# Optimization experiments

Measured on AMD Instinct MI355X. Metric: run time of the kernel, lower is better.

The kernel has to match this reference:

```python
import jax, jax.numpy as jnp
import numpy as np

N, D, K = 32768, 256, 4096
COMMITMENT_COST = 0.25
EPS_NORM = 1e-12  # matches torch F.normalize eps


def _l2_normalize(x):
    n = jnp.linalg.norm(x, axis=1, keepdims=True)
    return x / jnp.maximum(n, EPS_NORM)


def setup_inputs() -> dict:
    key = jax.random.key(0)
    k1, k2 = jax.random.split(key)
    inputs = jax.random.normal(k1, (N, D), dtype=jnp.float32)
    # xavier_uniform-like scale for the codebook
    bound = float(np.sqrt(6.0 / (K + D)))
    embeddings = jax.random.uniform(k2, (K, D), dtype=jnp.float32, minval=-bound, maxval=bound)
    return {"inputs": inputs, "embeddings": embeddings}


def reference(inputs, embeddings):
    flat = inputs.reshape(-1, D)
    x = _l2_normalize(flat)              # [N, D]
    e = _l2_normalize(embeddings)        # [K, D]
    # squared euclidean distance on normalized vectors
    distances = (jnp.sum(x * x, axis=1, keepdims=True)
                 + jnp.sum(e * e, axis=1)
                 - 2.0 * jnp.matmul(x, e.T))          # [N, K]
    encoding_indices = jnp.argmin(distances, axis=1)  # [N]
    quantized = embeddings[encoding_indices]          # gather, [N, D]
    # commitment loss (EMA variant: only commitment term is trained)
    e_latent_loss = jnp.mean((jax.lax.stop_gradient(quantized) - flat) ** 2)
    loss = COMMITMENT_COST * e_latent_loss
    # straight-through estimator
    quantized_st = flat + jax.lax.stop_gradient(quantized - flat)
    quantized_st = quantized_st.reshape(inputs.shape)
    return quantized_st, loss, encoding_indices
```

## Files before the change

kernel.cpp:

```cpp
#include <hip/hip_runtime.h>
#include <math.h>
#include <stdint.h>
#include <limits.h>

#define NPTS 32768
#define DIM  256
#define KCB  4096
#define NQ   (NPTS*DIM)

#define EPSN    1e-12f
#define MARGIN1 6.0e-4f
#define F16MIN  6.103515625e-05f
#define CAPB    4096
#define KINIT   0x7F800000FFFFFFFFull

typedef __attribute__((ext_vector_type(8))) _Float16 f16x8;
typedef __attribute__((ext_vector_type(4))) _Float16 f16x4;
typedef __attribute__((ext_vector_type(4))) float    f32x4;

#define WS_EH0   0u
#define WS_TRI   2097152u
#define WS_SUME  4194304u
#define WS_EINV  4210688u
#define WS_XINV  4227072u
#define WS_IDX   4358144u
#define WS_RCA   4489216u
#define WS_RLA   4489232u
#define WS_RCB   4751376u
#define WS_RLB   4751392u
#define WS_BEST  4882464u
#define WS_LOSSP 4915232u

__device__ inline unsigned fbits(float f){ union{float f;unsigned u;}v; v.f=f; return v.u; }
__device__ inline float bitsf(unsigned u){ union{float f;unsigned u;}v; v.u=u; return v.f; }
__device__ inline uint64_t dbits(double d){ union{double d;uint64_t u;}v; v.d=d; return v.u; }
__device__ inline _Float16 g16(float v){
    return (fabsf(v) < F16MIN) ? (_Float16)0.0f : (_Float16)v;
}
__device__ inline void gload16(const void* src, void* lds){
    __builtin_amdgcn_global_load_lds((const __attribute__((address_space(1))) void*)src,
                                     (__attribute__((address_space(3))) void*)lds, 16, 0, 0);
}

__global__ __launch_bounds__(256) void k_norm_x(const float* __restrict__ x,
                                                float* __restrict__ xinv) {
    int w = threadIdx.x >> 6, l = threadIdx.x & 63;
    int row = blockIdx.x * 4 + w;
    float4 v = ((const float4*)x)[row * 64 + l];
    float s = v.x*v.x + v.y*v.y + v.z*v.z + v.w*v.w;
    #pragma unroll
    for (int o = 32; o; o >>= 1) s += __shfl_xor(s, o);
    if (l == 0) xinv[row] = 1.0f / fmaxf(sqrtf(s), EPSN);
}

__global__ __launch_bounds__(256) void k_norm_e(const float* __restrict__ e,
                                                _Float16* __restrict__ eh0,
                                                float* __restrict__ sume,
                                                float* __restrict__ einv,
                                                int* __restrict__ rca,
                                                int* __restrict__ rcb,
                                                uint64_t* __restrict__ bestu) {
    if (blockIdx.x == 0 && threadIdx.x == 0) { *rca = 0; *rcb = 0; }
    if (blockIdx.x < 16) bestu[blockIdx.x * 256 + threadIdx.x] = ~0ull;
    int w = threadIdx.x >> 6, l = threadIdx.x & 63;
    int row = blockIdx.x * 4 + w;
    float4 v = ((const float4*)e)[row * 64 + l];
    float s = v.x*v.x + v.y*v.y + v.z*v.z + v.w*v.w;
    #pragma unroll
    for (int o = 32; o; o >>= 1) s += __shfl_xor(s, o);
    float inv = 1.0f / fmaxf(sqrtf(s), EPSN);
    float4 n = make_float4(v.x*inv, v.y*inv, v.z*inv, v.w*inv);
    f16x4 h0; h0[0]=g16(n.x); h0[1]=g16(n.y); h0[2]=g16(n.z); h0[3]=g16(n.w);
    ((f16x4*)eh0)[row * 64 + l] = h0;
    float s2 = n.x*n.x + n.y*n.y + n.z*n.z + n.w*n.w;
    #pragma unroll
    for (int o = 32; o; o >>= 1) s2 += __shfl_xor(s2, o);
    if (l == 0) { sume[row] = s2; einv[row] = inv; }
}

__global__ __launch_bounds__(256,2) void k_phase1(
    const float* __restrict__ x, const float* __restrict__ xinv,
    const _Float16* __restrict__ eh0,
    ulonglong2* __restrict__ tri)
{
    __shared__ __align__(16) _Float16 Bs[2][32 * DIM];
    const int tid = threadIdx.x;
    const int w = tid >> 6, l = tid & 63;
    const int l15 = l & 15, lhi = l >> 4;
    const int rowbase = (blockIdx.x >> 2) * 256 + w * 64;
    const int kbase   = (blockIdx.x & 3) * 1024;
    char* BsC = (char*)&Bs[0][0];

    f16x8 a[4][8];
    #pragma unroll
    for (int g = 0; g < 4; g++) {
        int row = rowbase + g*16 + l15;
        float xv = xinv[row];
        const float4* xr = (const float4*)(x + row * DIM);
        #pragma unroll
        for (int dc = 0; dc < 8; dc++) {
            float4 f0 = xr[dc*8 + lhi*2];
            float4 f1 = xr[dc*8 + lhi*2 + 1];
            f16x8 av;
            av[0]=g16(f0.x*xv); av[1]=g16(f0.y*xv);
            av[2]=g16(f0.z*xv); av[3]=g16(f0.w*xv);
            av[4]=g16(f1.x*xv); av[5]=g16(f1.y*xv);
            av[6]=g16(f1.z*xv); av[7]=g16(f1.w*xv);
            a[g][dc] = av;
        }
    }

    uint64_t t0[4], t1[4];
    float d2[4];
    #pragma unroll
    for (int g = 0; g < 4; g++) { t0[g]=KINIT; t1[g]=KINIT; d2[g]=INFINITY; }

    const char* sbase = (const char*)eh0 + (size_t)kbase * 512
                      + (size_t)(l & 31) * 512 + w*32 + (l >> 5)*16;
    auto stage = [&](int kt, int bufbyte) {
        const char* s = sbase + kt * 16384;
        #pragma unroll
        for (int p = 0; p < 4; p++) {
            gload16(s + p*128, BsC + bufbyte + ((p*256 + w*64) << 4));
        }
    };

    const int rb = lhi*512 + l15*16;
    const f32x4 zc = (f32x4){0.f, 0.f, 0.f, 0.f};

    auto compute = [&](int kt, int bufbyte) {
        f32x4 acc[4][2];
        #pragma unroll
        for (int dc = 0; dc < 8; dc++) {
            #pragma unroll
            for (int ni = 0; ni < 2; ni++) {
                f16x8 b = *(const f16x8*)(BsC + bufbyte + dc*2048 + ni*256 + rb);
                if (dc == 0) {
                    acc[0][ni] = __builtin_amdgcn_mfma_f32_16x16x32_f16(b, a[0][0], zc, 0, 0, 0);
                    acc[1][ni] = __builtin_amdgcn_mfma_f32_16x16x32_f16(b, a[1][0], zc, 0, 0, 0);
                    acc[2][ni] = __builtin_amdgcn_mfma_f32_16x16x32_f16(b, a[2][0], zc, 0, 0, 0);
                    acc[3][ni] = __builtin_amdgcn_mfma_f32_16x16x32_f16(b, a[3][0], zc, 0, 0, 0);
                } else {
                    acc[0][ni] = __builtin_amdgcn_mfma_f32_16x16x32_f16(b, a[0][dc], acc[0][ni], 0, 0, 0);
                    acc[1][ni] = __builtin_amdgcn_mfma_f32_16x16x32_f16(b, a[1][dc], acc[1][ni], 0, 0, 0);
                    acc[2][ni] = __builtin_amdgcn_mfma_f32_16x16x32_f16(b, a[2][dc], acc[2][ni], 0, 0, 0);
                    acc[3][ni] = __builtin_amdgcn_mfma_f32_16x16x32_f16(b, a[3][dc], acc[3][ni], 0, 0, 0);
                }
            }
        }

        #pragma unroll
        for (int ni = 0; ni < 2; ni++) {
            #pragma unroll
            for (int g = 0; g < 4; g++) {
                f32x4 v = acc[g][ni];
                float mx = fmaxf(fmaxf(v[0], v[1]), fmaxf(v[2], v[3]));
                if (5.0f - 2.0f*mx < d2[g]) {
                    #pragma unroll
                    for (int r = 0; r < 4; r++) {
                        float db = 5.0f - 2.0f*v[r];
                        if (db < d2[g]) {
                            int code = kbase + kt*32 + ni*16 + lhi*4 + r;
                            uint64_t key = ((uint64_t)fbits(db) << 32) | (unsigned)code;
                            if (key < t1[g]) {
                                d2[g] = bitsf((unsigned)(t1[g] >> 32));
                                if (key < t0[g]) { t1[g] = t0[g]; t0[g] = key; }
                                else t1[g] = key;
                            } else {
                                d2[g] = db;
                            }
                        }
                    }
                }
            }
        }
    };

    stage(0, 0);
    for (int kt = 0; kt < 32; kt += 2) {
        __syncthreads();
        stage(kt + 1, 16384);
        compute(kt, 0);
        __syncthreads();
        if (kt + 2 < 32) stage(kt + 2, 0);
        compute(kt + 1, 16384);
    }

    #pragma unroll
    for (int g = 0; g < 4; g++) {
        uint64_t a0 = t0[g], a1 = t1[g];
        float a2 = d2[g];
        #pragma unroll
        for (int m = 16; m < 64; m <<= 1) {
            uint64_t b0 = __shfl_xor(a0, m), b1 = __shfl_xor(a1, m);
            float    b2 = __shfl_xor(a2, m);
            uint64_t lo  = a0 < b0 ? a0 : b0;
            uint64_t hi0 = a0 < b0 ? b0 : a0;
            uint64_t lo1 = a1 < b1 ? a1 : b1;
            uint64_t mid = hi0 > lo1 ? hi0 : lo1;
            a1 = hi0 < lo1 ? hi0 : lo1;
            a0 = lo;
            a2 = fminf(fminf(a2, b2), bitsf((unsigned)(mid >> 32)));
        }
        t0[g] = a0; t1[g] = a1; d2[g] = a2;
    }

    if (lhi == 0) {
        const int split = blockIdx.x & 3;
        #pragma unroll
        for (int g = 0; g < 4; g++) {
            int row = rowbase + g*16 + l15;
            float d0 = bitsf((unsigned)(t0[g] >> 32));
            uint64_t flag = (d2[g] - d0 < MARGIN1) ? (1ull << 12) : 0ull;
            ulonglong2 ent;
            ent.x = t0[g];
            ent.y = t1[g] | flag;
            tri[(row << 2) | split] = ent;
        }
    }
}

__global__ __launch_bounds__(256) void k_merge(
    const ulonglong2* __restrict__ tri,
    int* __restrict__ idx,
    int* __restrict__ rca, int2* __restrict__ rla,
    int* __restrict__ rcb, int* __restrict__ rlb)
{
    int row = blockIdx.x * 256 + threadIdx.x;
    ulonglong2 e0 = tri[row*4 + 0];
    ulonglong2 e1 = tri[row*4 + 1];
    ulonglong2 e2 = tri[row*4 + 2];
    ulonglong2 e3 = tri[row*4 + 3];

    uint64_t c0 = e0.x, c1 = e0.y & ~0x1000ull;
    float c2 = INFINITY;
    auto fold = [&](uint64_t b0, uint64_t b1) {
        b1 &= ~0x1000ull;
        uint64_t lo  = c0 < b0 ? c0 : b0;
        uint64_t hi0 = c0 < b0 ? b0 : c0;
        uint64_t lo1 = c1 < b1 ? c1 : b1;
        uint64_t mid = hi0 > lo1 ? hi0 : lo1;
        c1 = hi0 < lo1 ? hi0 : lo1;
        c0 = lo;
        c2 = fminf(c2, bitsf((unsigned)(mid >> 32)));
    };
    fold(e1.x, e1.y);
    fold(e2.x, e2.y);
    fold(e3.x, e3.y);

    int k0 = (int)((unsigned)c0 & 0xFFFu);
    idx[row] = k0;
    float d0 = bitsf((unsigned)(c0 >> 32));
    float d1 = bitsf((unsigned)(c1 >> 32));
    bool lA = (d1 - d0 < MARGIN1);
    bool lB = (c2 - d0 < MARGIN1);
    if ((e0.y >> 12) & 1) lB |= (bitsf((unsigned)(e0.x >> 32)) - d0 < MARGIN1);
    if ((e1.y >> 12) & 1) lB |= (bitsf((unsigned)(e1.x >> 32)) - d0 < MARGIN1);
    if ((e2.y >> 12) & 1) lB |= (bitsf((unsigned)(e2.x >> 32)) - d0 < MARGIN1);
    if ((e3.y >> 12) & 1) lB |= (bitsf((unsigned)(e3.x >> 32)) - d0 < MARGIN1);

    if (lA) {
        int k1 = (int)((unsigned)c1 & 0xFFFu);
        int p = atomicAdd(rca, 1);
        if (p < NPTS) rla[p] = make_int2(row, k0 | (k1 << 12));
    }
    if (lB) {
        int q = atomicAdd(rcb, 1);
        if (q < CAPB) rlb[q] = row;
    }
}

__global__ __launch_bounds__(256) void k_cand(
    const float* __restrict__ x, const float* __restrict__ emb,
    const float* __restrict__ xinv, const float* __restrict__ einv,
    const float* __restrict__ sume,
    const int* __restrict__ rca, const int2* __restrict__ rla,
    int* __restrict__ idx)
{
    int cnt = *rca; if (cnt > NPTS) cnt = NPTS;
    const int w = threadIdx.x >> 6, l = threadIdx.x & 63;
    for (int r = blockIdx.x * 4 + w; r < cnt; r += gridDim.x * 4) {
        int2 ent = rla[r];
        int row = ent.x;
        int k0 = ent.y & 0xFFF, k1 = (ent.y >> 12) & 0xFFF;
        float xv = xinv[row];
        float4 xf = ((const float4*)x)[row * 64 + l];
        double x0 = (double)xf.x * (double)xv, x1 = (double)xf.y * (double)xv;
        double x2 = (double)xf.z * (double)xv, x3 = (double)xf.w * (double)xv;
        int ks[2] = {k0, k1};
        double d[2];
        #pragma unroll
        for (int c = 0; c < 2; c++) {
            int k = ks[c];
            float ev = einv[k];
            float4 e4 = ((const float4*)emb)[k * 64 + l];
            d[c] = x0 * (double)(e4.x * ev) + x1 * (double)(e4.y * ev)
                 + x2 * (double)(e4.z * ev) + x3 * (double)(e4.w * ev);
        }
        #pragma unroll
        for (int o = 32; o; o >>= 1) {
            d[0] += __shfl_xor(d[0], o);
            d[1] += __shfl_xor(d[1], o);
        }
        if (l == 0) {
            double dist0 = 4.0 + (double)sume[k0] - 2.0 * d[0];
            double dist1 = 4.0 + (double)sume[k1] - 2.0 * d[1];
            uint64_t key0 = (dbits(dist0) & 0xFFFFFFFFFFFFF000ull) | (unsigned)k0;
            uint64_t key1 = (dbits(dist1) & 0xFFFFFFFFFFFFF000ull) | (unsigned)k1;
            idx[row] = (int)((key0 < key1 ? key0 : key1) & 0xFFFull);
        }
    }
}

__global__ __launch_bounds__(256) void k_full(
    const float* __restrict__ x, const float* __restrict__ emb,
    const float* __restrict__ xinv, const float* __restrict__ einv,
    const float* __restrict__ sume,
    const int* __restrict__ rcb, const int* __restrict__ rlb,
    uint64_t* __restrict__ bestu)
{
    __shared__ __align__(16) float xs[DIM];
    int cnt = *rcb; if (cnt > CAPB) cnt = CAPB; if (cnt <= 0) return;
    const int tid = threadIdx.x;
    const int grp = tid >> 3, sub = tid & 7;
    int items = cnt * 16;
    for (int item = blockIdx.x; item < items; item += gridDim.x) {
        int r = item >> 4, chunk = item & 15;
        int row = rlb[r];
        __syncthreads();
        xs[tid] = x[row * DIM + tid] * xinv[row];
        __syncthreads();
        const float4* xs4 = (const float4*)xs;
        uint64_t best = ~0ull;
        #pragma unroll
        for (int j = 0; j < 8; j++) {
            int k = chunk * 256 + grp * 8 + j;
            float ev = einv[k];
            const float4* e4 = (const float4*)(emb + k * DIM);
            double dp = 0;
            #pragma unroll
            for (int i = 0; i < 8; i++) {
                float4 ef = e4[sub + i*8];
                float4 xf = xs4[sub + i*8];
                dp += (double)xf.x * (double)(ef.x * ev)
                    + (double)xf.y * (double)(ef.y * ev)
                    + (double)xf.z * (double)(ef.z * ev)
                    + (double)xf.w * (double)(ef.w * ev);
            }
            #pragma unroll
            for (int o = 4; o; o >>= 1) dp += __shfl_xor(dp, o);
            if (sub == 0) {
                double dist = 4.0 + (double)sume[k] - 2.0 * dp;
                uint64_t key = (dbits(dist) & 0xFFFFFFFFFFFFF000ull) | (unsigned)k;
                best = key < best ? key : best;
            }
        }
        if (sub == 0)
            atomicMin((unsigned long long*)&bestu[r], (unsigned long long)best);
    }
}

__global__ __launch_bounds__(256) void k_ffin(const int* __restrict__ rcb,
                                              const int* __restrict__ rlb,
                                              const uint64_t* __restrict__ bestu,
                                              int* __restrict__ idx) {
    int cnt = *rcb; if (cnt > CAPB) cnt = CAPB;
    int i = blockIdx.x * 256 + threadIdx.x;
    if (i < cnt) idx[rlb[i]] = (int)(bestu[i] & 0xFFFull);
}

__global__ __launch_bounds__(256) void k_gather(const float* __restrict__ x,
                                                const float* __restrict__ emb,
                                                const int* __restrict__ idx,
                                                float* __restrict__ out,
                                                float* __restrict__ lossp) {
    int t = blockIdx.x * 256 + threadIdx.x;
    float ls = 0.f;
    #pragma unroll
    for (int s = 0; s < 4; ++s) {
        int i4 = t + s * 524288;
        int n = i4 >> 6, c4 = i4 & 63;
        int id = idx[n];
        float4 f = ((const float4*)x)[i4];
        float4 q = ((const float4*)emb)[id * 64 + c4];
        float dx = q.x - f.x, dy = q.y - f.y, dz = q.z - f.z, dw = q.w - f.w;
        float4 o = make_float4(f.x + dx, f.y + dy, f.z + dz, f.w + dw);
        ((float4*)out)[i4] = o;
        ls += dx*dx + dy*dy + dz*dz + dw*dw;
        if (c4 == 0) out[NQ + 1 + n] = (float)id;
    }
    #pragma unroll
    for (int o = 32; o; o >>= 1) ls += __shfl_xor(ls, o);
    __shared__ float wsum[4];
    int wid = threadIdx.x >> 6, lane = threadIdx.x & 63;
    if (lane == 0) wsum[wid] = ls;
    __syncthreads();
    if (threadIdx.x == 0) lossp[blockIdx.x] = wsum[0] + wsum[1] + wsum[2] + wsum[3];
}

__global__ __launch_bounds__(256) void k_finalize(const float* __restrict__ lossp,
                                                  float* __restrict__ out) {
    double s = 0;
    for (int i = threadIdx.x; i < 2048; i += 256) s += (double)lossp[i];
    #pragma unroll
    for (int o = 32; o; o >>= 1) s += __shfl_xor(s, o);
    __shared__ double wd[4];
    int wid = threadIdx.x >> 6, lane = threadIdx.x & 63;
    if (lane == 0) wd[wid] = s;
    __syncthreads();
    if (threadIdx.x == 0)
        out[NQ] = (float)(0.25 * ((wd[0] + wd[1] + wd[2] + wd[3]) / (double)NQ));
}

extern "C" void kernel_launch(void* const* d_in, const int* in_sizes, int n_in,
                              void* d_out, int out_size, void* d_ws, size_t ws_size,
                              hipStream_t stream) {
    const float* x   = (const float*)d_in[0];
    const float* emb = (const float*)d_in[1];
    char* ws = (char*)d_ws;
    _Float16* eh0 = (_Float16*)(ws + WS_EH0);
    ulonglong2* tri = (ulonglong2*)(ws + WS_TRI);
    float* sume  = (float*)(ws + WS_SUME);
    float* einv  = (float*)(ws + WS_EINV);
    float* xinv  = (float*)(ws + WS_XINV);
    int*   idx   = (int*)  (ws + WS_IDX);
    int*   rca   = (int*)  (ws + WS_RCA);
    int2*  rla   = (int2*) (ws + WS_RLA);
    int*   rcb   = (int*)  (ws + WS_RCB);
    int*   rlb   = (int*)  (ws + WS_RLB);
    uint64_t* bestu = (uint64_t*)(ws + WS_BEST);
    float* lossp = (float*)(ws + WS_LOSSP);
    float* out = (float*)d_out;

    hipLaunchKernelGGL(k_norm_x,   dim3(NPTS/4),     dim3(256), 0, stream, x, xinv);
    hipLaunchKernelGGL(k_norm_e,   dim3(KCB/4),      dim3(256), 0, stream,
                       emb, eh0, sume, einv, rca, rcb, bestu);
    hipLaunchKernelGGL(k_phase1,   dim3(NPTS/256*4), dim3(256), 0, stream,
                       x, xinv, eh0, tri);
    hipLaunchKernelGGL(k_merge,    dim3(NPTS/256),   dim3(256), 0, stream,
                       tri, idx, rca, rla, rcb, rlb);
    hipLaunchKernelGGL(k_cand,     dim3(1024),       dim3(256), 0, stream,
                       x, emb, xinv, einv, sume, rca, rla, idx);
    hipLaunchKernelGGL(k_full,     dim3(2048),       dim3(256), 0, stream,
                       x, emb, xinv, einv, sume, rcb, rlb, bestu);
    hipLaunchKernelGGL(k_ffin,     dim3(16),         dim3(256), 0, stream, rcb, rlb, bestu, idx);
    hipLaunchKernelGGL(k_gather,   dim3(2048),       dim3(256), 0, stream,
                       x, emb, idx, out, lossp);
    hipLaunchKernelGGL(k_finalize, dim3(1),          dim3(256), 0, stream, lossp, out);
}
```

Measured before the change: 177.8 us.

## Fuse merge, candidate rescoring and full-rescan kernels into one block-local tail kernel

```diff
diff --git a/kernel.cpp b/kernel.cpp
--- a/kernel.cpp
+++ b/kernel.cpp
@@ -11,7 +11,6 @@
 #define EPSN    1e-12f
 #define MARGIN1 6.0e-4f
 #define F16MIN  6.103515625e-05f
-#define CAPB    4096
 #define KINIT   0x7F800000FFFFFFFFull
 
 typedef __attribute__((ext_vector_type(8))) _Float16 f16x8;
@@ -24,11 +23,6 @@
 #define WS_EINV  4210688u
 #define WS_XINV  4227072u
 #define WS_IDX   4358144u
-#define WS_RCA   4489216u
-#define WS_RLA   4489232u
-#define WS_RCB   4751376u
-#define WS_RLB   4751392u
-#define WS_BEST  4882464u
 #define WS_LOSSP 4915232u
 
 __device__ inline unsigned fbits(float f){ union{float f;unsigned u;}v; v.f=f; return v.u; }
@@ -56,12 +50,7 @@
 __global__ __launch_bounds__(256) void k_norm_e(const float* __restrict__ e,
                                                 _Float16* __restrict__ eh0,
                                                 float* __restrict__ sume,
-                                                float* __restrict__ einv,
-                                                int* __restrict__ rca,
-                                                int* __restrict__ rcb,
-                                                uint64_t* __restrict__ bestu) {
-    if (blockIdx.x == 0 && threadIdx.x == 0) { *rca = 0; *rcb = 0; }
-    if (blockIdx.x < 16) bestu[blockIdx.x * 256 + threadIdx.x] = ~0ull;
+                                                float* __restrict__ einv) {
     int w = threadIdx.x >> 6, l = threadIdx.x & 63;
     int row = blockIdx.x * 4 + w;
     float4 v = ((const float4*)e)[row * 64 + l];
@@ -220,69 +209,65 @@
     }
 }
 
-__global__ __launch_bounds__(256) void k_merge(
+__global__ __launch_bounds__(256) void k_tail(
     const ulonglong2* __restrict__ tri,
-    int* __restrict__ idx,
-    int* __restrict__ rca, int2* __restrict__ rla,
-    int* __restrict__ rcb, int* __restrict__ rlb)
-{
-    int row = blockIdx.x * 256 + threadIdx.x;
-    ulonglong2 e0 = tri[row*4 + 0];
-    ulonglong2 e1 = tri[row*4 + 1];
-    ulonglong2 e2 = tri[row*4 + 2];
-    ulonglong2 e3 = tri[row*4 + 3];
-
-    uint64_t c0 = e0.x, c1 = e0.y & ~0x1000ull;
-    float c2 = INFINITY;
-    auto fold = [&](uint64_t b0, uint64_t b1) {
-        b1 &= ~0x1000ull;
-        uint64_t lo  = c0 < b0 ? c0 : b0;
-        uint64_t hi0 = c0 < b0 ? b0 : c0;
-        uint64_t lo1 = c1 < b1 ? c1 : b1;
-        uint64_t mid = hi0 > lo1 ? hi0 : lo1;
-        c1 = hi0 < lo1 ? hi0 : lo1;
-        c0 = lo;
-        c2 = fminf(c2, bitsf((unsigned)(mid >> 32)));
-    };
-    fold(e1.x, e1.y);
-    fold(e2.x, e2.y);
-    fold(e3.x, e3.y);
-
-    int k0 = (int)((unsigned)c0 & 0xFFFu);
-    idx[row] = k0;
-    float d0 = bitsf((unsigned)(c0 >> 32));
-    float d1 = bitsf((unsigned)(c1 >> 32));
-    bool lA = (d1 - d0 < MARGIN1);
-    bool lB = (c2 - d0 < MARGIN1);
-    if ((e0.y >> 12) & 1) lB |= (bitsf((unsigned)(e0.x >> 32)) - d0 < MARGIN1);
-    if ((e1.y >> 12) & 1) lB |= (bitsf((unsigned)(e1.x >> 32)) - d0 < MARGIN1);
-    if ((e2.y >> 12) & 1) lB |= (bitsf((unsigned)(e2.x >> 32)) - d0 < MARGIN1);
-    if ((e3.y >> 12) & 1) lB |= (bitsf((unsigned)(e3.x >> 32)) - d0 < MARGIN1);
-
-    if (lA) {
-        int k1 = (int)((unsigned)c1 & 0xFFFu);
-        int p = atomicAdd(rca, 1);
-        if (p < NPTS) rla[p] = make_int2(row, k0 | (k1 << 12));
-    }
-    if (lB) {
-        int q = atomicAdd(rcb, 1);
-        if (q < CAPB) rlb[q] = row;
-    }
-}
-
-__global__ __launch_bounds__(256) void k_cand(
     const float* __restrict__ x, const float* __restrict__ emb,
     const float* __restrict__ xinv, const float* __restrict__ einv,
     const float* __restrict__ sume,
-    const int* __restrict__ rca, const int2* __restrict__ rla,
     int* __restrict__ idx)
 {
-    int cnt = *rca; if (cnt > NPTS) cnt = NPTS;
-    const int w = threadIdx.x >> 6, l = threadIdx.x & 63;
-    for (int r = blockIdx.x * 4 + w; r < cnt; r += gridDim.x * 4) {
-        int2 ent = rla[r];
-        int row = ent.x;
-        int k0 = ent.y & 0xFFF, k1 = (ent.y >> 12) & 0xFFF;
+    __shared__ int rowsA[256], ksA[256], rowsB[256];
+    __shared__ int cntA, cntB;
+    __shared__ __align__(16) float xs[DIM];
+    __shared__ uint64_t sk[32];
+    const int tid = threadIdx.x;
+    if (tid == 0) { cntA = 0; cntB = 0; }
+    __syncthreads();
+
+    {
+        int row = blockIdx.x * 256 + tid;
+        ulonglong2 e0 = tri[row*4+0], e1 = tri[row*4+1],
+                   e2 = tri[row*4+2], e3 = tri[row*4+3];
+        uint64_t c0 = e0.x, c1 = e0.y & ~0x1000ull;
+        float c2 = INFINITY;
+        auto fold = [&](uint64_t b0, uint64_t b1) {
+            b1 &= ~0x1000ull;
+            uint64_t lo  = c0 < b0 ? c0 : b0;
+            uint64_t hi0 = c0 < b0 ? b0 : c0;
+            uint64_t lo1 = c1 < b1 ? c1 : b1;
+            uint64_t mid = hi0 > lo1 ? hi0 : lo1;
+            c1 = hi0 < lo1 ? hi0 : lo1;
+            c0 = lo;
+            c2 = fminf(c2, bitsf((unsigned)(mid >> 32)));
+        };
+        fold(e1.x, e1.y); fold(e2.x, e2.y); fold(e3.x, e3.y);
+        int k0 = (int)((unsigned)c0 & 0xFFFu);
+        idx[row] = k0;
+        float d0 = bitsf((unsigned)(c0 >> 32));
+        float d1 = bitsf((unsigned)(c1 >> 32));
+        bool lA = (d1 - d0 < MARGIN1);
+        bool lB = (c2 - d0 < MARGIN1);
+        if ((e0.y >> 12) & 1) lB |= (bitsf((unsigned)(e0.x >> 32)) - d0 < MARGIN1);
+        if ((e1.y >> 12) & 1) lB |= (bitsf((unsigned)(e1.x >> 32)) - d0 < MARGIN1);
+        if ((e2.y >> 12) & 1) lB |= (bitsf((unsigned)(e2.x >> 32)) - d0 < MARGIN1);
+        if ((e3.y >> 12) & 1) lB |= (bitsf((unsigned)(e3.x >> 32)) - d0 < MARGIN1);
+        if (lA) {
+            int k1 = (int)((unsigned)c1 & 0xFFFu);
+            int p = atomicAdd(&cntA, 1);
+            rowsA[p] = row; ksA[p] = k0 | (k1 << 12);
+        }
+        if (lB) {
+            int q = atomicAdd(&cntB, 1);
+            rowsB[q] = row;
+        }
+    }
+    __syncthreads();
+
+    const int w = tid >> 6, l = tid & 63;
+    const int nA = cntA;
+    for (int i = w; i < nA; i += 4) {
+        int row = rowsA[i];
+        int k0 = ksA[i] & 0xFFF, k1 = (ksA[i] >> 12) & 0xFFF;
         float xv = xinv[row];
         float4 xf = ((const float4*)x)[row * 64 + l];
         double x0 = (double)xf.x * (double)xv, x1 = (double)xf.y * (double)xv;
@@ -310,38 +295,27 @@
             idx[row] = (int)((key0 < key1 ? key0 : key1) & 0xFFFull);
         }
     }
-}
-
-__global__ __launch_bounds__(256) void k_full(
-    const float* __restrict__ x, const float* __restrict__ emb,
-    const float* __restrict__ xinv, const float* __restrict__ einv,
-    const float* __restrict__ sume,
-    const int* __restrict__ rcb, const int* __restrict__ rlb,
-    uint64_t* __restrict__ bestu)
-{
-    __shared__ __align__(16) float xs[DIM];
-    int cnt = *rcb; if (cnt > CAPB) cnt = CAPB; if (cnt <= 0) return;
-    const int tid = threadIdx.x;
+    __syncthreads();
+
+    const int nB = cntB;
     const int grp = tid >> 3, sub = tid & 7;
-    int items = cnt * 16;
-    for (int item = blockIdx.x; item < items; item += gridDim.x) {
-        int r = item >> 4, chunk = item & 15;
-        int row = rlb[r];
+    for (int i = 0; i < nB; i++) {
+        int brow = rowsB[i];
         __syncthreads();
-        xs[tid] = x[row * DIM + tid] * xinv[row];
+        xs[tid] = x[brow * DIM + tid] * xinv[brow];
+        if (tid < 32) sk[tid] = ~0ull;
         __syncthreads();
         const float4* xs4 = (const float4*)xs;
         uint64_t best = ~0ull;
-        #pragma unroll
-        for (int j = 0; j < 8; j++) {
-            int k = chunk * 256 + grp * 8 + j;
+        for (int j = 0; j < 128; j++) {
+            int k = grp * 128 + j;
             float ev = einv[k];
-            const float4* e4 = (const float4*)(emb + k * DIM);
+            const float4* e4 = (const float4*)(emb + (size_t)k * DIM);
             double dp = 0;
             #pragma unroll
-            for (int i = 0; i < 8; i++) {
-                float4 ef = e4[sub + i*8];
-                float4 xf = xs4[sub + i*8];
+            for (int ii = 0; ii < 8; ii++) {
+                float4 ef = e4[sub + ii*8];
+                float4 xf = xs4[sub + ii*8];
                 dp += (double)xf.x * (double)(ef.x * ev)
                     + (double)xf.y * (double)(ef.y * ev)
                     + (double)xf.z * (double)(ef.z * ev)
@@ -355,18 +329,14 @@
                 best = key < best ? key : best;
             }
         }
-        if (sub == 0)
-            atomicMin((unsigned long long*)&bestu[r], (unsigned long long)best);
-    }
-}
-
-__global__ __launch_bounds__(256) void k_ffin(const int* __restrict__ rcb,
-                                              const int* __restrict__ rlb,
-                                              const uint64_t* __restrict__ bestu,
-                                              int* __restrict__ idx) {
-    int cnt = *rcb; if (cnt > CAPB) cnt = CAPB;
-    int i = blockIdx.x * 256 + threadIdx.x;
-    if (i < cnt) idx[rlb[i]] = (int)(bestu[i] & 0xFFFull);
+        if (sub == 0) sk[grp] = best;
+        __syncthreads();
+        if (tid == 0) {
+            uint64_t b = sk[0];
+            for (int gg = 1; gg < 32; gg++) b = sk[gg] < b ? sk[gg] : b;
+            idx[brow] = (int)(b & 0xFFFull);
+        }
+    }
 }
 
 __global__ __launch_bounds__(256) void k_gather(const float* __restrict__ x,
@@ -424,26 +394,16 @@
     float* einv  = (float*)(ws + WS_EINV);
     float* xinv  = (float*)(ws + WS_XINV);
     int*   idx   = (int*)  (ws + WS_IDX);
-    int*   rca   = (int*)  (ws + WS_RCA);
-    int2*  rla   = (int2*) (ws + WS_RLA);
-    int*   rcb   = (int*)  (ws + WS_RCB);
-    int*   rlb   = (int*)  (ws + WS_RLB);
-    uint64_t* bestu = (uint64_t*)(ws + WS_BEST);
     float* lossp = (float*)(ws + WS_LOSSP);
     float* out = (float*)d_out;
 
     hipLaunchKernelGGL(k_norm_x,   dim3(NPTS/4),     dim3(256), 0, stream, x, xinv);
     hipLaunchKernelGGL(k_norm_e,   dim3(KCB/4),      dim3(256), 0, stream,
-                       emb, eh0, sume, einv, rca, rcb, bestu);
+                       emb, eh0, sume, einv);
     hipLaunchKernelGGL(k_phase1,   dim3(NPTS/256*4), dim3(256), 0, stream,
                        x, xinv, eh0, tri);
-    hipLaunchKernelGGL(k_merge,    dim3(NPTS/256),   dim3(256), 0, stream,
-                       tri, idx, rca, rla, rcb, rlb);
-    hipLaunchKernelGGL(k_cand,     dim3(1024),       dim3(256), 0, stream,
-                       x, emb, xinv, einv, sume, rca, rla, idx);
-    hipLaunchKernelGGL(k_full,     dim3(2048),       dim3(256), 0, stream,
-                       x, emb, xinv, einv, sume, rcb, rlb, bestu);
-    hipLaunchKernelGGL(k_ffin,     dim3(16),         dim3(256), 0, stream, rcb, rlb, bestu, idx);
+    hipLaunchKernelGGL(k_tail,     dim3(NPTS/256),   dim3(256), 0, stream,
+                       tri, x, emb, xinv, einv, sume, idx);
     hipLaunchKernelGGL(k_gather,   dim3(2048),       dim3(256), 0, stream,
                        x, emb, idx, out, lossp);
     hipLaunchKernelGGL(k_finalize, dim3(1),          dim3(256), 0, stream, lossp, out);
```

Measured after the change: 335.3 us. 1.89x slower.
